# Performance work log

Measured on AMD Instinct MI355X. Metric: run time of the kernel, lower is better.

## Reference

```python
import jax, jax.numpy as jnp
import numpy as np

DIM = 96
HEADS = 8  # num_heads_v
EPS = 1e-12  # torch F.normalize eps


def conv1x1(x, w, b):
    # x: [B,C,H,W], w: [O,C,1,1], b: [O]
    y = jnp.einsum('bchw,oc->bohw', x, w[:, :, 0, 0])
    return y + b[None, :, None, None]


def dwconv3x3(x, w, b):
    # depthwise 3x3, groups == channels; w: [C,1,3,3]
    y = jax.lax.conv_general_dilated(
        x, w, window_strides=(1, 1), padding=((1, 1), (1, 1)),
        dimension_numbers=('NCHW', 'OIHW', 'NCHW'),
        feature_group_count=x.shape[1])
    return y + b[None, :, None, None]


def setup_inputs() -> dict:
    key = jax.random.key(0)
    ks = jax.random.split(key, 7)
    c = DIM
    s = 0.05
    x = jax.random.normal(ks[0], (4, c, 256, 256), jnp.float32)
    qkv_w = jax.random.normal(ks[1], (3 * c, c, 1, 1), jnp.float32) * s
    qkv_b = jax.random.normal(ks[2], (3 * c,), jnp.float32) * s
    dw_w = jax.random.normal(ks[3], (3 * c, 1, 3, 3), jnp.float32) * s
    dw_b = jax.random.normal(ks[4], (3 * c,), jnp.float32) * s
    proj_w = jax.random.normal(ks[5], (c, c, 1, 1), jnp.float32) * s
    proj_b = jax.random.normal(ks[6], (c,), jnp.float32) * s
    temperature = jnp.ones((HEADS, 1, 1), jnp.float32)
    return {"x": x, "qkv_w": qkv_w, "qkv_b": qkv_b, "dw_w": dw_w,
            "dw_b": dw_b, "proj_w": proj_w, "proj_b": proj_b,
            "temperature": temperature}


def reference(x, qkv_w, qkv_b, dw_w, dw_b, proj_w, proj_b, temperature):
    b, c, h, w = x.shape
    head = temperature.shape[0]
    w2 = w // head
    qkv = dwconv3x3(conv1x1(x, qkv_w, qkv_b), dw_w, dw_b)
    q0, k0, v0 = jnp.split(qkv, 3, axis=1)  # each [b,c,h,w]

    def to_heads(t):
        # 'b c h (head w2) -> b head w2 (c h)'
        t = t.reshape(b, c, h, head, w2)
        return jnp.transpose(t, (0, 3, 4, 1, 2)).reshape(b, head, w2, c * h)

    q = to_heads(q0)
    k = to_heads(k0)
    v = to_heads(v0)
    q = q / jnp.maximum(jnp.linalg.norm(q, axis=-1, keepdims=True), EPS)
    k = k / jnp.maximum(jnp.linalg.norm(k, axis=-1, keepdims=True), EPS)
    attn = jnp.einsum('bhid,bhjd->bhij', q, k) * temperature[None]  # [b,head,w2,w2]
    attn = jax.nn.softmax(attn, axis=-1)
    out = jnp.einsum('bhij,bhjd->bhid', attn, v)  # [b,head,w2,c*h]
    # 'b head w2 (c h) -> b c h (head w2)'
    out = out.reshape(b, head, w2, c, h)
    out = jnp.transpose(out, (0, 3, 4, 1, 2)).reshape(b, c, h, w)
    return conv1x1(out, proj_w, proj_b)
```

## Files before the change

### kernel.cpp

```cpp
#include <hip/hip_runtime.h>

#define CC 96
#define C3 288
#define HH 256
#define WW 256
#define HWC 65536
#define NHEADS 8
#define W2 32

typedef __bf16 bf16x8 __attribute__((ext_vector_type(8)));
typedef float f32x4 __attribute__((ext_vector_type(4)));
typedef unsigned short us8v __attribute__((ext_vector_type(8)));

__device__ __forceinline__ float bf2f(unsigned short u) {
  return __uint_as_float(((unsigned)u) << 16);
}
__device__ __forceinline__ unsigned short f2bf(float f) {
  unsigned u = __float_as_uint(f);
  unsigned r = u + 0x7fffu + ((u >> 16) & 1u);
  return (unsigned short)(r >> 16);
}

__global__ __launch_bounds__(256, 4) void k1_qkv_mfma(
    const float* __restrict__ x, const float* __restrict__ qw,
    const float* __restrict__ qb, unsigned short* __restrict__ pre, int b0)
{
  __shared__ __align__(16) unsigned short As2[2][64 * 106];
  const int t = threadIdx.x;
  const int o0 = blockIdx.x * 96;
  const int bz = blockIdx.z;
  const float* xb = x + (size_t)(b0 + bz) * CC * HWC;

  const int wave = t >> 6, lane = t & 63;
  const int wm = wave & 1, wn = wave >> 1;
  const int row = lane & 15, kg = lane >> 4;

  bf16x8 bfr[3][3];
  float bias[3];
#pragma unroll
  for (int nt = 0; nt < 3; ++nt) {
    int ocl = wn * 48 + nt * 16 + row;
    bias[nt] = qb[o0 + ocl];
#pragma unroll
    for (int kk = 0; kk < 3; ++kk) {
      const float* wp = qw + (size_t)(o0 + ocl) * 96 + kk * 32 + kg * 8;
      float4 w0 = *reinterpret_cast<const float4*>(wp);
      float4 w1 = *reinterpret_cast<const float4*>(wp + 4);
      us8v u;
      u[0] = f2bf(w0.x); u[1] = f2bf(w0.y); u[2] = f2bf(w0.z); u[3] = f2bf(w0.w);
      u[4] = f2bf(w1.x); u[5] = f2bf(w1.y); u[6] = f2bf(w1.z); u[7] = f2bf(w1.w);
      bfr[kk][nt] = *reinterpret_cast<bf16x8*>(&u);
    }
  }

  int sic[3], sp4[3];
#pragma unroll
  for (int r = 0; r < 3; ++r) {
    int lin = r * 256 + t;
    sic[r] = lin >> 4;
    sp4[r] = (lin & 15) * 4;
  }

  int p0 = blockIdx.y * 512;
  float4 va0[3], va1[3];
#pragma unroll
  for (int r = 0; r < 3; ++r) {
    va0[r] = *reinterpret_cast<const float4*>(xb + (size_t)(2 * sic[r]) * HWC + p0 + sp4[r]);
    va1[r] = *reinterpret_cast<const float4*>(xb + (size_t)(2 * sic[r] + 1) * HWC + p0 + sp4[r]);
  }

  for (int i = 0; i < 8; ++i) {
    unsigned short* Ac = As2[i & 1];
#pragma unroll
    for (int r = 0; r < 3; ++r) {
      float a0[4] = {va0[r].x, va0[r].y, va0[r].z, va0[r].w};
      float a1[4] = {va1[r].x, va1[r].y, va1[r].z, va1[r].w};
#pragma unroll
      for (int j = 0; j < 4; ++j) {
        unsigned pk = (unsigned)f2bf(a0[j]) | ((unsigned)f2bf(a1[j]) << 16);
        *reinterpret_cast<unsigned*>(&Ac[(sp4[r] + j) * 106 + 2 * sic[r]]) = pk;
      }
    }
    if (i < 7) {
      int p0n = p0 + 64;
#pragma unroll
      for (int r = 0; r < 3; ++r) {
        va0[r] = *reinterpret_cast<const float4*>(xb + (size_t)(2 * sic[r]) * HWC + p0n + sp4[r]);
        va1[r] = *reinterpret_cast<const float4*>(xb + (size_t)(2 * sic[r] + 1) * HWC + p0n + sp4[r]);
      }
    }
    __syncthreads();

    f32x4 acc[2][3];
#pragma unroll
    for (int mt = 0; mt < 2; ++mt)
#pragma unroll
      for (int nt = 0; nt < 3; ++nt) acc[mt][nt] = (f32x4){0.f, 0.f, 0.f, 0.f};
#pragma unroll
    for (int kk = 0; kk < 3; ++kk) {
      bf16x8 a[2];
#pragma unroll
      for (int mt = 0; mt < 2; ++mt)
        a[mt] = *reinterpret_cast<const bf16x8*>(
            &Ac[(wm * 32 + mt * 16 + row) * 106 + kk * 32 + kg * 8]);
#pragma unroll
      for (int mt = 0; mt < 2; ++mt)
#pragma unroll
        for (int nt = 0; nt < 3; ++nt)
          acc[mt][nt] = __builtin_amdgcn_mfma_f32_16x16x32_bf16(
              a[mt], bfr[kk][nt], acc[mt][nt], 0, 0, 0);
    }
    __syncthreads();

    unsigned short* tD = (unsigned short*)As2;
#pragma unroll
    for (int nt = 0; nt < 3; ++nt) {
      int ocl = wn * 48 + nt * 16 + row;
      float bv = bias[nt];
#pragma unroll
      for (int mt = 0; mt < 2; ++mt) {
        int pxl = wm * 32 + mt * 16 + kg * 4;
        f32x4 v = acc[mt][nt];
        unsigned pk0 = (unsigned)f2bf(v[0] + bv) | ((unsigned)f2bf(v[1] + bv) << 16);
        unsigned pk1 = (unsigned)f2bf(v[2] + bv) | ((unsigned)f2bf(v[3] + bv) << 16);
        *reinterpret_cast<unsigned*>(&tD[ocl * 72 + pxl]) = pk0;
        *reinterpret_cast<unsigned*>(&tD[ocl * 72 + pxl + 2]) = pk1;
      }
    }
    __syncthreads();
    unsigned short* preb = pre + ((size_t)bz * C3 + o0) * HWC + p0;
#pragma unroll
    for (int r = 0; r < 3; ++r) {
      int lin = r * 256 + t;
      int oc = lin >> 3, ch = lin & 7;
      us8v v = *reinterpret_cast<const us8v*>(&tD[oc * 72 + ch * 8]);
      *reinterpret_cast<us8v*>(preb + (size_t)oc * HWC + ch * 8) = v;
    }
    __syncthreads();
    p0 += 64;
  }
}

__global__ __launch_bounds__(256) void k2_dw(
    const unsigned short* __restrict__ pre, const float* __restrict__ dww,
    const float* __restrict__ dwb, unsigned short* __restrict__ dwo)
{
  const int t = threadIdx.x;
  const int c3 = blockIdx.x;
  const int hb = blockIdx.y;
  const int bz = blockIdx.z;
  const size_t choff = ((size_t)bz * C3 + c3) * HWC;
  const int team = t >> 5, tl = t & 31;
  const int h0 = hb * 32 + team * 4;

  us8v rin[6];
#pragma unroll
  for (int r = 0; r < 6; ++r) {
    int hh = h0 - 1 + r;
    if (hh >= 0 && hh < HH)
      rin[r] = *reinterpret_cast<const us8v*>(pre + choff + (size_t)hh * WW + tl * 8);
    else
      rin[r] = (us8v){0, 0, 0, 0, 0, 0, 0, 0};
  }

  float wg[9];
#pragma unroll
  for (int i = 0; i < 9; ++i) wg[i] = dww[c3 * 9 + i];
  const float bias = dwb[c3];

  float f[6][8];
  float lf[6], rt[6];
#pragma unroll
  for (int r = 0; r < 6; ++r) {
#pragma unroll
    for (int j = 0; j < 8; ++j) f[r][j] = bf2f(rin[r][j]);
    float l = __shfl_up(f[r][7], 1, 32);
    float rr = __shfl_down(f[r][0], 1, 32);
    lf[r] = (tl == 0) ? 0.f : l;
    rt[r] = (tl == 31) ? 0.f : rr;
  }

#pragma unroll
  for (int orow = 0; orow < 4; ++orow) {
    float o[8];
#pragma unroll
    for (int j = 0; j < 8; ++j) o[j] = bias;
#pragma unroll
    for (int k = 0; k < 3; ++k) {
      const int r = orow + k;
      const float w0 = wg[k * 3 + 0], w1 = wg[k * 3 + 1], w2 = wg[k * 3 + 2];
      o[0] = fmaf(lf[r], w0, fmaf(f[r][0], w1, fmaf(f[r][1], w2, o[0])));
#pragma unroll
      for (int j = 1; j < 7; ++j)
        o[j] = fmaf(f[r][j - 1], w0, fmaf(f[r][j], w1, fmaf(f[r][j + 1], w2, o[j])));
      o[7] = fmaf(f[r][6], w0, fmaf(f[r][7], w1, fmaf(rt[r], w2, o[7])));
    }
    us8v u;
#pragma unroll
    for (int j = 0; j < 8; ++j) u[j] = f2bf(o[j]);
    *reinterpret_cast<us8v*>((unsigned short*)dwo + choff + (size_t)(h0 + orow) * WW + tl * 8) = u;
  }
}

__global__ __launch_bounds__(256, 4) void k3_gram(
    const unsigned short* __restrict__ dwo, float* __restrict__ gpart,
    float* __restrict__ ssq)
{
  __shared__ __align__(16) unsigned short qT[32 * 264];
  __shared__ __align__(16) unsigned short kT[32 * 264];
  const int t = threadIdx.x;
  const int cg0 = blockIdx.x;
  const int head = blockIdx.y, bz = blockIdx.z;
  const int lane = t & 63, wave = t >> 6;
  const int mt = wave & 1, nt = wave >> 1;
  const int l15 = lane & 15, l4 = lane >> 4;
  const int cg = t & 7;
  int rp[4];
#pragma unroll
  for (int r = 0; r < 4; ++r) rp[r] = (r * 256 + t) >> 3;

  const unsigned short* qbase = dwo + ((size_t)bz * C3 + cg0 * 4) * HWC + head * W2;
  const unsigned short* kbase = qbase + (size_t)CC * HWC;

  ushort4 qa[4], qb_[4], ka[4], kb_[4];
#pragma unroll
  for (int r = 0; r < 4; ++r) {
    qa[r] = *reinterpret_cast<const ushort4*>(qbase + (size_t)(2 * rp[r]) * WW + cg * 4);
    qb_[r] = *reinterpret_cast<const ushort4*>(qbase + (size_t)(2 * rp[r] + 1) * WW + cg * 4);
    ka[r] = *reinterpret_cast<const ushort4*>(kbase + (size_t)(2 * rp[r]) * WW + cg * 4);
    kb_[r] = *reinterpret_cast<const ushort4*>(kbase + (size_t)(2 * rp[r] + 1) * WW + cg * 4);
  }

  f32x4 acc = (f32x4){0.f, 0.f, 0.f, 0.f};
  float ssum_q = 0.f, ssum_k = 0.f;

  for (int cc = 0; cc < 4; ++cc) {
#pragma unroll
    for (int r = 0; r < 4; ++r) {
      unsigned short aq0[4] = {qa[r].x, qa[r].y, qa[r].z, qa[r].w};
      unsigned short aq1[4] = {qb_[r].x, qb_[r].y, qb_[r].z, qb_[r].w};
      unsigned short ak0[4] = {ka[r].x, ka[r].y, ka[r].z, ka[r].w};
      unsigned short ak1[4] = {kb_[r].x, kb_[r].y, kb_[r].z, kb_[r].w};
#pragma unroll
      for (int j = 0; j < 4; ++j) {
        int dwi = (cg * 4 + j) * 132 + rp[r];
        *(reinterpret_cast<unsigned*>(qT) + dwi) =
            (unsigned)aq0[j] | ((unsigned)aq1[j] << 16);
        *(reinterpret_cast<unsigned*>(kT) + dwi) =
            (unsigned)ak0[j] | ((unsigned)ak1[j] << 16);
      }
    }
    if (cc < 3) {
      const unsigned short* qn = qbase + (size_t)(cc + 1) * HWC;
      const unsigned short* kn = kbase + (size_t)(cc + 1) * HWC;
#pragma unroll
      for (int r = 0; r < 4; ++r) {
        qa[r] = *reinterpret_cast<const ushort4*>(qn + (size_t)(2 * rp[r]) * WW + cg * 4);
        qb_[r] = *reinterpret_cast<const ushort4*>(qn + (size_t)(2 * rp[r] + 1) * WW + cg * 4);
        ka[r] = *reinterpret_cast<const ushort4*>(kn + (size_t)(2 * rp[r]) * WW + cg * 4);
        kb_[r] = *reinterpret_cast<const ushort4*>(kn + (size_t)(2 * rp[r] + 1) * WW + cg * 4);
      }
    }
    __builtin_amdgcn_sched_barrier(0);
    __syncthreads();
#pragma unroll
    for (int kk = 0; kk < 8; ++kk) {
      bf16x8 a = *reinterpret_cast<const bf16x8*>(
          &qT[(mt * 16 + l15) * 264 + kk * 32 + l4 * 8]);
      bf16x8 b = *reinterpret_cast<const bf16x8*>(
          &kT[(nt * 16 + l15) * 264 + kk * 32 + l4 * 8]);
      acc = __builtin_amdgcn_mfma_f32_16x16x32_bf16(a, b, acc, 0, 0, 0);
    }
    {
      const int i = t & 31, seg = t >> 5;
#pragma unroll
      for (int m = 0; m < 4; ++m) {
        us8v vq = *reinterpret_cast<const us8v*>(&qT[i * 264 + seg * 32 + m * 8]);
        us8v vk = *reinterpret_cast<const us8v*>(&kT[i * 264 + seg * 32 + m * 8]);
#pragma unroll
        for (int e = 0; e < 8; ++e) {
          float fq = bf2f(vq[e]), fk = bf2f(vk[e]);
          ssum_q = fmaf(fq, fq, ssum_q);
          ssum_k = fmaf(fk, fk, ssum_k);
        }
      }
    }
    __syncthreads();
  }

  float* gp = gpart + (((size_t)bz * NHEADS + head) * 24 + cg0) * 1024;
#pragma unroll
  for (int reg = 0; reg < 4; ++reg)
    gp[(nt * 16 + l15) * 32 + mt * 16 + l4 * 4 + reg] = acc[reg];

  float* red = reinterpret_cast<float*>(qT);
  red[t] = ssum_q;
  red[256 + t] = ssum_k;
  __syncthreads();
  if (t < 32) {
    float sq = 0.f, sk = 0.f;
#pragma unroll
    for (int p = 0; p < 8; ++p) { sq += red[t + 32 * p]; sk += red[256 + t + 32 * p]; }
    atomicAdd(&ssq[(size_t)bz * 512 + head * W2 + t], sq);
    atomicAdd(&ssq[(size_t)bz * 512 + 256 + head * W2 + t], sk);
  }
}

__global__ __launch_bounds__(256) void k4b_softmax(
    const float* __restrict__ gpart, const float* __restrict__ ssq,
    const float* __restrict__ temp, float* __restrict__ attn)
{
  __shared__ float lg[1024];
  const int t = threadIdx.x;
  const int head = blockIdx.x, bz = blockIdx.y;
  const float* gp = gpart + ((size_t)bz * NHEADS + head) * 24 * 1024;
  float4 s = make_float4(0.f, 0.f, 0.f, 0.f);
#pragma unroll 4
  for (int cg = 0; cg < 24; ++cg) {
    float4 v = *reinterpret_cast<const float4*>(gp + cg * 1024 + t * 4);
    s.x += v.x; s.y += v.y; s.z += v.z; s.w += v.w;
  }
  *reinterpret_cast<float4*>(&lg[t * 4]) = s;
  __syncthreads();
  if (t < 32) {
    const int i = t;
    const float* sq_ = ssq + (size_t)bz * 512 + head * W2;
    const float* sk_ = ssq + (size_t)bz * 512 + 256 + head * W2;
    float invq = 1.f / fmaxf(sqrtf(sq_[i]), 1e-12f);
    float tpq = temp[head] * invq;
    float rowv[32];
    float m = -1e30f;
#pragma unroll
    for (int j = 0; j < 32; ++j) {
      float invk = 1.f / fmaxf(sqrtf(sk_[j]), 1e-12f);
      float v = lg[j * 32 + i] * tpq * invk;
      rowv[j] = v;
      m = fmaxf(m, v);
    }
    float ssum = 0;
#pragma unroll
    for (int j = 0; j < 32; ++j) { rowv[j] = expf(rowv[j] - m); ssum += rowv[j]; }
    float inv = 1.f / ssum;
    float* ap = attn + ((size_t)bz * NHEADS + head) * 1024 + i * 32;
#pragma unroll
    for (int j = 0; j < 32; ++j) ap[j] = rowv[j] * inv;
  }
}

__global__ __launch_bounds__(256) void k5a_attnv(
    const unsigned short* __restrict__ dwo, const float* __restrict__ attn,
    unsigned short* __restrict__ tbuf)
{
  __shared__ __align__(16) unsigned short vsm[64 * 264];
  __shared__ __align__(16) unsigned short atn_s[256 * 36];
  const int t = threadIdx.x;
  const int tile = blockIdx.x;
  const int bz = blockIdx.y;
  const size_t R0 = (size_t)tile * 64;
  const unsigned short* vsrc = dwo + ((size_t)bz * C3 + 2 * CC) * HWC + R0 * 256;

  us8v vv[8];
#pragma unroll
  for (int j = 0; j < 8; ++j)
    vv[j] = *reinterpret_cast<const us8v*>(vsrc + (size_t)(j * 256 + t) * 8);
  float4 av[8];
  {
    const float* ap = attn + (size_t)bz * 8192 + t * 32;
#pragma unroll
    for (int k = 0; k < 8; ++k)
      av[k] = *reinterpret_cast<const float4*>(ap + k * 4);
  }
  __builtin_amdgcn_sched_barrier(0);
#pragma unroll
  for (int j = 0; j < 8; ++j) {
    int n = j * 256 + t;
    int row = n >> 5, c8 = n & 31;
    *reinterpret_cast<us8v*>(&vsm[row * 264 + c8 * 8]) = vv[j];
  }
#pragma unroll
  for (int k = 0; k < 8; ++k) {
    ushort4 u;
    u.x = f2bf(av[k].x); u.y = f2bf(av[k].y); u.z = f2bf(av[k].z); u.w = f2bf(av[k].w);
    *reinterpret_cast<ushort4*>(&atn_s[t * 36 + k * 4]) = u;
  }
  __syncthreads();

  const int wave = t >> 6, lane = t & 63;
  const int mrow = lane & 15, kg = lane >> 4;

  bf16x8 a[8], b[16];
#pragma unroll
  for (int hd = 0; hd < 8; ++hd)
    a[hd] = *reinterpret_cast<const bf16x8*>(
        &vsm[(wave * 16 + mrow) * 264 + hd * 32 + kg * 8]);
#pragma unroll
  for (int hd = 0; hd < 8; ++hd)
#pragma unroll
    for (int it = 0; it < 2; ++it)
      b[hd * 2 + it] = *reinterpret_cast<const bf16x8*>(
          &atn_s[(hd * 32 + it * 16 + mrow) * 36 + kg * 8]);

  f32x4 acc[16];
#pragma unroll
  for (int q = 0; q < 16; ++q) acc[q] = (f32x4){0.f, 0.f, 0.f, 0.f};
#pragma unroll
  for (int hd = 0; hd < 8; ++hd)
#pragma unroll
    for (int it = 0; it < 2; ++it)
      acc[hd * 2 + it] = __builtin_amdgcn_mfma_f32_16x16x32_bf16(
          a[hd], b[hd * 2 + it], acc[hd * 2 + it], 0, 0, 0);
  __syncthreads();

#pragma unroll
  for (int hd = 0; hd < 8; ++hd)
#pragma unroll
    for (int it = 0; it < 2; ++it) {
      f32x4 v = acc[hd * 2 + it];
      int col = hd * 32 + it * 16 + mrow;
#pragma unroll
      for (int r = 0; r < 4; ++r)
        vsm[(wave * 16 + kg * 4 + r) * 264 + col] = f2bf(v[r]);
    }
  unsigned short* tdst = tbuf + (size_t)bz * CC * HWC + R0 * 256;
#pragma unroll
  for (int k = 0; k < 8; ++k) {
    int n = k * 64 + lane;
    int rloc = n >> 5, c8 = n & 31;
    us8v v = *reinterpret_cast<const us8v*>(&vsm[(wave * 16 + rloc) * 264 + c8 * 8]);
    *reinterpret_cast<us8v*>(tdst + ((size_t)(wave * 16 + rloc)) * 256 + c8 * 8) = v;
  }
}

__global__ __launch_bounds__(256, 4) void k5b_proj(
    const unsigned short* __restrict__ tbuf, const float* __restrict__ pw,
    const float* __restrict__ pb, float* __restrict__ out, int b0)
{
  __shared__ __align__(16) unsigned short As2[2][64 * 106];
  const int t = threadIdx.x;
  const int bz = blockIdx.y;
  const unsigned short* tb = tbuf + (size_t)bz * CC * HWC;

  const int wave = t >> 6, lane = t & 63;
  const int wm = wave & 1, wn = wave >> 1;
  const int row = lane & 15, kg = lane >> 4;

  bf16x8 bfr[3][3];
  float bias[3];
#pragma unroll
  for (int nt = 0; nt < 3; ++nt) {
    int ocl = wn * 48 + nt * 16 + row;
    bias[nt] = pb[ocl];
#pragma unroll
    for (int kk = 0; kk < 3; ++kk) {
      const float* wp = pw + (size_t)ocl * 96 + kk * 32 + kg * 8;
      float4 w0 = *reinterpret_cast<const float4*>(wp);
      float4 w1 = *reinterpret_cast<const float4*>(wp + 4);
      us8v u;
      u[0] = f2bf(w0.x); u[1] = f2bf(w0.y); u[2] = f2bf(w0.z); u[3] = f2bf(w0.w);
      u[4] = f2bf(w1.x); u[5] = f2bf(w1.y); u[6] = f2bf(w1.z); u[7] = f2bf(w1.w);
      bfr[kk][nt] = *reinterpret_cast<bf16x8*>(&u);
    }
  }

  int sic[3], sp4[3];
#pragma unroll
  for (int r = 0; r < 3; ++r) {
    int lin = r * 256 + t;
    sic[r] = lin >> 4;
    sp4[r] = (lin & 15) * 4;
  }

  int p0 = blockIdx.x * 512;
  ushort4 ua0[3], ua1[3];
#pragma unroll
  for (int r = 0; r < 3; ++r) {
    ua0[r] = *reinterpret_cast<const ushort4*>(tb + (size_t)(2 * sic[r]) * HWC + p0 + sp4[r]);
    ua1[r] = *reinterpret_cast<const ushort4*>(tb + (size_t)(2 * sic[r] + 1) * HWC + p0 + sp4[r]);
  }

  for (int i = 0; i < 8; ++i) {
    unsigned short* Ac = As2[i & 1];
#pragma unroll
    for (int r = 0; r < 3; ++r) {
      unsigned short a0[4] = {ua0[r].x, ua0[r].y, ua0[r].z, ua0[r].w};
      unsigned short a1[4] = {ua1[r].x, ua1[r].y, ua1[r].z, ua1[r].w};
#pragma unroll
      for (int j = 0; j < 4; ++j) {
        unsigned pk = (unsigned)a0[j] | ((unsigned)a1[j] << 16);
        *reinterpret_cast<unsigned*>(&Ac[(sp4[r] + j) * 106 + 2 * sic[r]]) = pk;
      }
    }
    if (i < 7) {
      int p0n = p0 + 64;
#pragma unroll
      for (int r = 0; r < 3; ++r) {
        ua0[r] = *reinterpret_cast<const ushort4*>(tb + (size_t)(2 * sic[r]) * HWC + p0n + sp4[r]);
        ua1[r] = *reinterpret_cast<const ushort4*>(tb + (size_t)(2 * sic[r] + 1) * HWC + p0n + sp4[r]);
      }
    }
    __syncthreads();

    f32x4 acc[2][3];
#pragma unroll
    for (int mt = 0; mt < 2; ++mt)
#pragma unroll
      for (int nt = 0; nt < 3; ++nt) acc[mt][nt] = (f32x4){0.f, 0.f, 0.f, 0.f};
#pragma unroll
    for (int kk = 0; kk < 3; ++kk) {
      bf16x8 a[2];
#pragma unroll
      for (int mt = 0; mt < 2; ++mt)
        a[mt] = *reinterpret_cast<const bf16x8*>(
            &Ac[(wm * 32 + mt * 16 + row) * 106 + kk * 32 + kg * 8]);
#pragma unroll
      for (int mt = 0; mt < 2; ++mt)
#pragma unroll
        for (int nt = 0; nt < 3; ++nt)
          acc[mt][nt] = __builtin_amdgcn_mfma_f32_16x16x32_bf16(
              a[mt], bfr[kk][nt], acc[mt][nt], 0, 0, 0);
    }
    __syncthreads();

    float* tD = (float*)As2;
#pragma unroll
    for (int nt = 0; nt < 3; ++nt) {
      int ocl = wn * 48 + nt * 16 + row;
      float bv = bias[nt];
#pragma unroll
      for (int mt = 0; mt < 2; ++mt) {
        int pxl = wm * 32 + mt * 16 + kg * 4;
        f32x4 v = acc[mt][nt];
        float4 w = make_float4(v[0] + bv, v[1] + bv, v[2] + bv, v[3] + bv);
        *reinterpret_cast<float4*>(&tD[ocl * 68 + pxl]) = w;
      }
    }
    __syncthreads();
    float* ob = out + (size_t)(b0 + bz) * CC * HWC + p0;
#pragma unroll
    for (int r = 0; r < 6; ++r) {
      int lin = r * 256 + t;
      int o = lin >> 4, p4 = (lin & 15) * 4;
      float4 v = *reinterpret_cast<const float4*>(&tD[o * 68 + p4]);
      *reinterpret_cast<float4*>(ob + (size_t)o * HWC + p4) = v;
    }
    __syncthreads();
    p0 += 64;
  }
}

extern "C" void kernel_launch(void* const* d_in, const int* in_sizes, int n_in,
                              void* d_out, int out_size, void* d_ws, size_t ws_size,
                              hipStream_t stream)
{
  const float* x      = (const float*)d_in[0];
  const float* qkv_w  = (const float*)d_in[1];
  const float* qkv_b  = (const float*)d_in[2];
  const float* dw_w   = (const float*)d_in[3];
  const float* dw_b   = (const float*)d_in[4];
  const float* proj_w = (const float*)d_in[5];
  const float* proj_b = (const float*)d_in[6];
  const float* temp   = (const float*)d_in[7];
  float* out = (float*)d_out;

  const size_t per_pre   = (size_t)C3 * HWC * 2;
  const size_t per_ssq   = (size_t)2 * 256 * 4;
  const size_t per_attn  = (size_t)NHEADS * 1024 * 4;
  const size_t per_gpart = (size_t)NHEADS * 24 * 1024 * 4;
  const size_t per_b = per_pre * 2 + per_ssq + per_attn + per_gpart;

  int bc = 4;
  while (bc > 1 && per_b * (size_t)bc > ws_size) bc >>= 1;

  char* p = (char*)d_ws;
  unsigned short* pre = (unsigned short*)p; p += per_pre * bc;
  unsigned short* dwo = (unsigned short*)p; p += per_pre * bc;
  float* ssq   = (float*)p; p += per_ssq * bc;
  float* attn  = (float*)p; p += per_attn * bc;
  float* gpart = (float*)p; p += per_gpart * bc;
  unsigned short* tbuf = pre;

  for (int b0 = 0; b0 < 4; b0 += bc) {
    k1_qkv_mfma<<<dim3(3, 128, bc), 256, 0, stream>>>(x, qkv_w, qkv_b, pre, b0);
    k2_dw<<<dim3(C3, 8, bc), 256, 0, stream>>>(pre, dw_w, dw_b, dwo);
    hipMemsetAsync(ssq, 0, per_ssq * bc, stream);
    k3_gram<<<dim3(24, NHEADS, bc), 256, 0, stream>>>(dwo, gpart, ssq);
    k4b_softmax<<<dim3(NHEADS, bc), 256, 0, stream>>>(gpart, ssq, temp, attn);
    k5a_attnv<<<dim3(384, bc), 256, 0, stream>>>(dwo, attn, tbuf);
    k5b_proj<<<dim3(128, bc), 256, 0, stream>>>(tbuf, proj_w, proj_b, out, b0);
  }
}
```

Measured before the change: 232.8 us.

## Fuse V depthwise conv into attn-V kernel and drop V intermediate buffer

The depthwise 3x3 conv for the V channels moves out of k2_dw and is recomputed inside k5a_attnv, which reads V from the pointwise-conv output and convolves into shared memory. The dw output buffer shrinks to Q and K only, removing a full write and re-read of the V tensor. tbuf gets its own workspace slot because pre is still needed as input. k1's grid axes are also swapped so consecutive blocks walk pixel tiles instead of output-channel groups. The cost is extra halo reads and conv arithmetic inside the attention kernel.

```diff
diff --git a/kernel.cpp b/kernel.cpp
--- a/kernel.cpp
+++ b/kernel.cpp
@@ -27,7 +27,7 @@
 {
   __shared__ __align__(16) unsigned short As2[2][64 * 106];
   const int t = threadIdx.x;
-  const int o0 = blockIdx.x * 96;
+  const int o0 = blockIdx.y * 96;
   const int bz = blockIdx.z;
   const float* xb = x + (size_t)(b0 + bz) * CC * HWC;
 
@@ -61,7 +61,7 @@
     sp4[r] = (lin & 15) * 4;
   }
 
-  int p0 = blockIdx.y * 512;
+  int p0 = blockIdx.x * 512;
   float4 va0[3], va1[3];
 #pragma unroll
   for (int r = 0; r < 3; ++r) {
@@ -149,7 +149,8 @@
   const int c3 = blockIdx.x;
   const int hb = blockIdx.y;
   const int bz = blockIdx.z;
-  const size_t choff = ((size_t)bz * C3 + c3) * HWC;
+  const size_t choff_in  = ((size_t)bz * C3 + c3) * HWC;
+  const size_t choff_out = ((size_t)bz * 192 + c3) * HWC;
   const int team = t >> 5, tl = t & 31;
   const int h0 = hb * 32 + team * 4;
 
@@ -158,7 +159,7 @@
   for (int r = 0; r < 6; ++r) {
     int hh = h0 - 1 + r;
     if (hh >= 0 && hh < HH)
-      rin[r] = *reinterpret_cast<const us8v*>(pre + choff + (size_t)hh * WW + tl * 8);
+      rin[r] = *reinterpret_cast<const us8v*>(pre + choff_in + (size_t)hh * WW + tl * 8);
     else
       rin[r] = (us8v){0, 0, 0, 0, 0, 0, 0, 0};
   }
@@ -198,7 +199,7 @@
     us8v u;
 #pragma unroll
     for (int j = 0; j < 8; ++j) u[j] = f2bf(o[j]);
-    *reinterpret_cast<us8v*>((unsigned short*)dwo + choff + (size_t)(h0 + orow) * WW + tl * 8) = u;
+    *reinterpret_cast<us8v*>((unsigned short*)dwo + choff_out + (size_t)(h0 + orow) * WW + tl * 8) = u;
   }
 }
 
@@ -219,7 +220,7 @@
 #pragma unroll
   for (int r = 0; r < 4; ++r) rp[r] = (r * 256 + t) >> 3;
 
-  const unsigned short* qbase = dwo + ((size_t)bz * C3 + cg0 * 4) * HWC + head * W2;
+  const unsigned short* qbase = dwo + ((size_t)bz * 192 + cg0 * 4) * HWC + head * W2;
   const unsigned short* kbase = qbase + (size_t)CC * HWC;
 
   ushort4 qa[4], qb_[4], ka[4], kb_[4];
@@ -348,7 +349,8 @@
 }
 
 __global__ __launch_bounds__(256) void k5a_attnv(
-    const unsigned short* __restrict__ dwo, const float* __restrict__ attn,
+    const unsigned short* __restrict__ pre, const float* __restrict__ dww,
+    const float* __restrict__ dwb, const float* __restrict__ attn,
     unsigned short* __restrict__ tbuf)
 {
   __shared__ __align__(16) unsigned short vsm[64 * 264];
@@ -357,12 +359,11 @@
   const int tile = blockIdx.x;
   const int bz = blockIdx.y;
   const size_t R0 = (size_t)tile * 64;
-  const unsigned short* vsrc = dwo + ((size_t)bz * C3 + 2 * CC) * HWC + R0 * 256;
-
-  us8v vv[8];
-#pragma unroll
-  for (int j = 0; j < 8; ++j)
-    vv[j] = *reinterpret_cast<const us8v*>(vsrc + (size_t)(j * 256 + t) * 8);
+  const int c = tile >> 2;
+  const int h0 = (tile & 3) * 64;
+  const unsigned short* vsrc = pre + ((size_t)bz * C3 + 2 * CC + c) * HWC;
+  const int team = t >> 5, tl = t & 31;
+
   float4 av[8];
   {
     const float* ap = attn + (size_t)bz * 8192 + t * 32;
@@ -370,12 +371,55 @@
     for (int k = 0; k < 8; ++k)
       av[k] = *reinterpret_cast<const float4*>(ap + k * 4);
   }
-  __builtin_amdgcn_sched_barrier(0);
-#pragma unroll
-  for (int j = 0; j < 8; ++j) {
-    int n = j * 256 + t;
-    int row = n >> 5, c8 = n & 31;
-    *reinterpret_cast<us8v*>(&vsm[row * 264 + c8 * 8]) = vv[j];
+
+  float wg[9];
+#pragma unroll
+  for (int i = 0; i < 9; ++i) wg[i] = dww[(2 * CC + c) * 9 + i];
+  const float vbias = dwb[2 * CC + c];
+
+#pragma unroll
+  for (int p = 0; p < 2; ++p) {
+    const int hb = h0 + team * 8 + p * 4;
+    us8v rin[6];
+#pragma unroll
+    for (int r = 0; r < 6; ++r) {
+      int hh = hb - 1 + r;
+      if (hh >= 0 && hh < HH)
+        rin[r] = *reinterpret_cast<const us8v*>(vsrc + (size_t)hh * WW + tl * 8);
+      else
+        rin[r] = (us8v){0, 0, 0, 0, 0, 0, 0, 0};
+    }
+    float f[6][8], lf[6], rt[6];
+#pragma unroll
+    for (int r = 0; r < 6; ++r) {
+#pragma unroll
+      for (int j = 0; j < 8; ++j) f[r][j] = bf2f(rin[r][j]);
+      float l = __shfl_up(f[r][7], 1, 32);
+      float rr = __shfl_down(f[r][0], 1, 32);
+      lf[r] = (tl == 0) ? 0.f : l;
+      rt[r] = (tl == 31) ? 0.f : rr;
+    }
+#pragma unroll
+    for (int orow = 0; orow < 4; ++orow) {
+      float o[8];
+#pragma unroll
+      for (int j = 0; j < 8; ++j) o[j] = vbias;
+#pragma unroll
+      for (int k = 0; k < 3; ++k) {
+        const int r = orow + k;
+        const float w0 = wg[k * 3 + 0], w1 = wg[k * 3 + 1], w2 = wg[k * 3 + 2];
+        o[0] = fmaf(lf[r], w0, fmaf(f[r][0], w1, fmaf(f[r][1], w2, o[0])));
+#pragma unroll
+        for (int j = 1; j < 7; ++j)
+          o[j] = fmaf(f[r][j - 1], w0, fmaf(f[r][j], w1, fmaf(f[r][j + 1], w2, o[j])));
+        o[7] = fmaf(f[r][6], w0, fmaf(f[r][7], w1, fmaf(rt[r], w2, o[7])));
+      }
+      us8v u;
+#pragma unroll
+      for (int j = 0; j < 8; ++j) u[j] = f2bf(o[j]);
+      int rl = team * 8 + p * 4 + orow;
+      *reinterpret_cast<us8v*>(&vsm[rl * 264 + tl * 8]) = u;
+    }
   }
 #pragma unroll
   for (int k = 0; k < 8; ++k) {
@@ -563,29 +607,31 @@
   float* out = (float*)d_out;
 
   const size_t per_pre   = (size_t)C3 * HWC * 2;
+  const size_t per_dwo   = (size_t)192 * HWC * 2;
+  const size_t per_tbuf  = (size_t)CC * HWC * 2;
   const size_t per_ssq   = (size_t)2 * 256 * 4;
   const size_t per_attn  = (size_t)NHEADS * 1024 * 4;
   const size_t per_gpart = (size_t)NHEADS * 24 * 1024 * 4;
-  const size_t per_b = per_pre * 2 + per_ssq + per_attn + per_gpart;
+  const size_t per_b = per_pre + per_dwo + per_tbuf + per_ssq + per_attn + per_gpart;
 
   int bc = 4;
   while (bc > 1 && per_b * (size_t)bc > ws_size) bc >>= 1;
 
   char* p = (char*)d_ws;
-  unsigned short* pre = (unsigned short*)p; p += per_pre * bc;
-  unsigned short* dwo = (unsigned short*)p; p += per_pre * bc;
+  unsigned short* pre  = (unsigned short*)p; p += per_pre * bc;
+  unsigned short* dwo  = (unsigned short*)p; p += per_dwo * bc;
+  unsigned short* tbuf = (unsigned short*)p; p += per_tbuf * bc;
   float* ssq   = (float*)p; p += per_ssq * bc;
   float* attn  = (float*)p; p += per_attn * bc;
   float* gpart = (float*)p; p += per_gpart * bc;
-  unsigned short* tbuf = pre;
 
   for (int b0 = 0; b0 < 4; b0 += bc) {
-    k1_qkv_mfma<<<dim3(3, 128, bc), 256, 0, stream>>>(x, qkv_w, qkv_b, pre, b0);
-    k2_dw<<<dim3(C3, 8, bc), 256, 0, stream>>>(pre, dw_w, dw_b, dwo);
+    k1_qkv_mfma<<<dim3(128, 3, bc), 256, 0, stream>>>(x, qkv_w, qkv_b, pre, b0);
+    k2_dw<<<dim3(192, 8, bc), 256, 0, stream>>>(pre, dw_w, dw_b, dwo);
     hipMemsetAsync(ssq, 0, per_ssq * bc, stream);
     k3_gram<<<dim3(24, NHEADS, bc), 256, 0, stream>>>(dwo, gpart, ssq);
     k4b_softmax<<<dim3(NHEADS, bc), 256, 0, stream>>>(gpart, ssq, temp, attn);
-    k5a_attnv<<<dim3(384, bc), 256, 0, stream>>>(dwo, attn, tbuf);
+    k5a_attnv<<<dim3(384, bc), 256, 0, stream>>>(pre, dw_w, dw_b, attn, tbuf);
     k5b_proj<<<dim3(128, bc), 256, 0, stream>>>(tbuf, proj_w, proj_b, out, b0);
   }
 }
```

New measurement: 223.2 us. 1.04x faster.
